# Optimization experiments

Measured on AMD Instinct MI355X. Metric: run time of the kernel, lower is better.

The kernel has to match this reference:

```python
import jax, jax.numpy as jnp
import numpy as np

B, S, HID, NH = 1, 2048, 2048, 16
HD = HID // NH
HALF = HD // 2
# quantization scales (registered buffers / pack() scales in the original module)
ATTN_IN_SCALE = 0.02   # attn_input_scale: dequant scale of int8 hidden_states
Q_OUT_SCALE = 0.05     # q_output_scale
K_OUT_SCALE = 0.05     # k_output_scale
V_OUT_SCALE = 0.04     # v_output_scale
Q_ROT_SCALE = 0.06     # q_rotary_output_scale
K_ROT_SCALE = 0.06     # k_rotary_output_scale
OUT_IN_SCALE = 0.03    # out_input_scale
W_ALPHA = 0.002        # folded int8 GEMM alpha for q/k/v W8A8B8O8Linear
BETA = 1.0             # bias scale of W8A8B8O8Linear
O_ALPHA = 0.001        # folded alpha for o_proj W8A8BFP32OFP32Linear
PROB_SCALE = 1.0 / 127.0  # attention-prob int8 quant scale
INV_SQRT_HD = float(1.0 / np.sqrt(HD))


def _q8(x):
    # saturating int8 quantization (values kept in float32)
    return jnp.clip(jnp.round(x), -127.0, 127.0)


def setup_inputs() -> dict:
    key = jax.random.key(0)
    ks = jax.random.split(key, 10)
    hidden_states = jax.random.normal(ks[0], (B, S, HID), jnp.float32)
    pos = jnp.arange(S, dtype=jnp.float32)
    inv_freq = 1.0 / (10000.0 ** (jnp.arange(0, HD, 2, dtype=jnp.float32) / HD))
    freqs = pos[:, None] * inv_freq[None, :]          # (S, HD//2)
    cos, sin = jnp.cos(freqs), jnp.sin(freqs)
    w8 = lambda k: jax.random.randint(k, (HID, HID), -127, 128).astype(jnp.float32)
    b8 = lambda k: jax.random.randint(k, (HID,), -127, 128).astype(jnp.float32)
    return dict(
        hidden_states=hidden_states, cos=cos, sin=sin,
        wq=w8(ks[1]), wk=w8(ks[2]), wv=w8(ks[3]), wo=w8(ks[4]),
        bq=b8(ks[5]), bk=b8(ks[6]), bv=b8(ks[7]),
        bo=jax.random.normal(ks[8], (HID,), jnp.float32) * 0.01,
    )


def reference(hidden_states, cos, sin, wq, wk, wv, wo, bq, bk, bv, bo):
    # quantize activations to int8 (done upstream of the module in smoothquant)
    x8 = _q8(hidden_states / ATTN_IN_SCALE)                       # (B,S,HID) int8 vals

    # W8A8B8O8Linear: int8 GEMM, alpha-scaled, int8 bias, saturate to int8
    def lin8(x, w, b):
        return _q8(jnp.einsum('bsi,oi->bso', x, w) * W_ALPHA + BETA * b)

    q8, k8, v8 = lin8(x8, wq, bq), lin8(x8, wk, bk), lin8(x8, wv, bv)

    # int8_rotary_embedding_fwd: dequant -> split-half rotary -> requant
    def rope(x8_flat, in_scale, out_scale):
        x = x8_flat.reshape(B, S, NH, HD) * in_scale
        x0, x1 = x[..., :HALF], x[..., HALF:]
        c, s_ = cos[None, :, None, :], sin[None, :, None, :]
        rot = jnp.concatenate([x0 * c - x1 * s_, x0 * s_ + x1 * c], axis=-1)
        return _q8(rot / out_scale)

    q = rope(q8, Q_OUT_SCALE, Q_ROT_SCALE)                        # (B,S,NH,HD)
    k = rope(k8, K_OUT_SCALE, K_ROT_SCALE)
    v = v8.reshape(B, S, NH, HD)

    # smooth_llama_context_attn_fwd: int8 QK^T -> fp32 scores -> causal softmax
    scores = jnp.einsum('bqhd,bkhd->bhqk', q, k) * (Q_ROT_SCALE * K_ROT_SCALE * INV_SQRT_HD)
    causal = jnp.tril(jnp.ones((S, S), bool))
    scores = jnp.where(causal[None, None], scores, -1e9)
    p = jax.nn.softmax(scores, axis=-1)
    p8 = _q8(p * 127.0)                                           # quantize probs to int8
    # int8 PV bmm, rescale and saturate to int8 for o_proj input
    o8 = _q8(jnp.einsum('bhqk,bkhd->bqhd', p8, v) * (PROB_SCALE * V_OUT_SCALE / OUT_IN_SCALE))
    o8 = o8.reshape(B, S, HID)

    # W8A8BFP32OFP32Linear: int8 GEMM, fp32 alpha + fp32 bias
    out = jnp.einsum('bso,po->bsp', o8, wo) * O_ALPHA + bo
    return out
```

## Files before the change

kernel.cpp:

```cpp
#include <hip/hip_runtime.h>
#include <math.h>

typedef __attribute__((ext_vector_type(4))) int i32x4;
typedef signed char s8;

constexpr int S   = 2048;
constexpr int HID = 2048;
constexpr int NH  = 16;
constexpr int HD  = 128;
constexpr int HALF = 64;

#define SCORE_SCALE ((float)(0.06 * 0.06 * 0.08838834764831845))
#define OSCALE      ((float)(((1.0 / 127.0) * 0.04) / 0.03))

__device__ __forceinline__ float clip127(float r){
  return fminf(fmaxf(r, -127.0f), 127.0f);
}
__device__ __forceinline__ i32x4 mfma_i8(i32x4 a, i32x4 b, i32x4 c){
  return __builtin_amdgcn_mfma_i32_16x16x64_i8(a, b, c, 0, 0, 0);
}
__device__ __forceinline__ void async16(const void* g, void* l){
  __builtin_amdgcn_global_load_lds(
      (const __attribute__((address_space(1))) unsigned*)g,
      (__attribute__((address_space(3))) unsigned*)l, 16, 0, 0);
}
template<int ROWS>
__device__ __forceinline__ void stage_async_swz(s8* dst, const s8* src, int stride){
  const int tid = threadIdx.x;
#pragma unroll
  for (int i = 0; i < ROWS/32; ++i){
    int o = i*256 + tid;
    int row = o >> 3, ch = o & 7;
    async16(src + (size_t)row*stride + ((ch ^ (row & 7))*16), dst + o*16);
  }
}
__device__ __forceinline__ i32x4 rd16(const s8* buf, int row, int ch){
  return *(const i32x4*)(buf + row*128 + ((ch ^ (row & 7))*16));
}
template<int ROWS>
__device__ __forceinline__ void stage64(s8* dst, const s8* src, int stride){
  const int tid = threadIdx.x;
#pragma unroll
  for (int i = 0; i < ROWS/64; ++i){
    int o = i*256 + tid;
    int row = o >> 2, slot = o & 3;
    int ch = slot ^ ((row >> 2) & 3);
    async16(src + (size_t)row*stride + ch*16, dst + o*16);
  }
}
__device__ __forceinline__ i32x4 rd64(const s8* buf, int row, int g){
  return *(const i32x4*)(buf + row*64 + ((g ^ ((row >> 2) & 3))*16));
}
__device__ __forceinline__ int tri_qt(int t){
  int qt = (int)((sqrtf(8.f*t + 1.f) - 1.f)*0.5f);
  while ((qt+1)*(qt+2)/2 <= t) ++qt;
  while (qt*(qt+1)/2 > t) --qt;
  return qt;
}

__global__ void cvt_all(const float* __restrict__ hid, const float* __restrict__ wq,
                        const float* __restrict__ wk, const float* __restrict__ wv,
                        const float* __restrict__ wo, s8* __restrict__ xd,
                        s8* __restrict__ qd, s8* __restrict__ kd,
                        s8* __restrict__ vd, s8* __restrict__ od, int n){
  const float* srcs[5] = {hid, wq, wk, wv, wo};
  s8* dsts[5] = {xd, qd, kd, vd, od};
  int which = blockIdx.y;
  const float* src = srcs[which];
  s8* dst = dsts[which];
  int i = (blockIdx.x * blockDim.x + threadIdx.x) * 4;
  if (i >= n) return;
  float4 v = *(const float4*)(src + i);
  float x[4] = {v.x, v.y, v.z, v.w};
  unsigned packed = 0;
#pragma unroll
  for (int j = 0; j < 4; ++j){
    int b;
    if (which == 0) b = (int)clip127(rintf(x[j] / 0.02f));
    else            b = (int)x[j];
    packed |= ((unsigned)(b & 255)) << (8*j);
  }
  *(unsigned*)(dst + i) = packed;
}

__global__ __launch_bounds__(256)
void gemm_qkv(const s8* __restrict__ A, const s8* __restrict__ W,
              const float* __restrict__ bq, const float* __restrict__ bk,
              const float* __restrict__ bv, s8* __restrict__ Out){
#pragma clang fp contract(off)
  constexpr int Kd = 2048, N = 2048, NT = 32;
  const int z = blockIdx.z;
  const s8* Bt = W + (size_t)z*(4u<<20);
  s8* Y = Out + (size_t)z*(4u<<20);
  const float* bss[3] = {bq, bk, bv};
  const float* bias = bss[z];
  __shared__ __attribute__((aligned(16))) s8 As[3][128*64];
  __shared__ __attribute__((aligned(16))) s8 Bs[3][128*64];
  const int lin = blockIdx.x + (blockIdx.y << 4);
  const int virt = (lin & 7)*32 + (lin >> 3);
  const int bm = virt & 15, bn = virt >> 4;
  const int tid = threadIdx.x;
  const int wid = tid >> 6, lane = tid & 63;
  const int wm = wid >> 1, wn = wid & 1;
  const int col16 = lane & 15, g = lane >> 4;
  i32x4 acc[4][4] = {};
  const s8* Ab = A + (size_t)(bm*128)*Kd;
  const s8* Bb = Bt + (size_t)(bn*128)*Kd;

  stage64<128>(As[0], Ab, Kd);       stage64<128>(Bs[0], Bb, Kd);
  stage64<128>(As[1], Ab + 64, Kd);  stage64<128>(Bs[1], Bb + 64, Kd);
  asm volatile("s_waitcnt vmcnt(4)" ::: "memory");
  __builtin_amdgcn_s_barrier();

  for (int T = 0; T < NT; ++T){
    const int nxt = T + 2;
    if (nxt < NT){
      stage64<128>(As[nxt%3], Ab + nxt*64, Kd);
      stage64<128>(Bs[nxt%3], Bb + nxt*64, Kd);
    }
    const s8* as = As[T%3];
    const s8* bs = Bs[T%3];
    i32x4 af[4], bf[4];
#pragma unroll
    for (int i = 0; i < 4; ++i) af[i] = rd64(as, wm*64 + i*16 + col16, g);
#pragma unroll
    for (int j = 0; j < 4; ++j) bf[j] = rd64(bs, wn*64 + j*16 + col16, g);
#pragma unroll
    for (int i = 0; i < 4; ++i)
#pragma unroll
      for (int j = 0; j < 4; ++j)
        acc[i][j] = mfma_i8(af[i], bf[j], acc[i][j]);
    if (nxt < NT) asm volatile("s_waitcnt vmcnt(4)" ::: "memory");
    else          asm volatile("s_waitcnt vmcnt(0)" ::: "memory");
    __builtin_amdgcn_s_barrier();
  }

#pragma unroll
  for (int i = 0; i < 4; ++i){
#pragma unroll
    for (int j = 0; j < 4; ++j){
      int row0 = bm*128 + wm*64 + i*16 + g*4;
      int col  = bn*128 + wn*64 + j*16 + col16;
#pragma unroll
      for (int r = 0; r < 4; ++r){
        float t = (float)acc[i][j][r] * 0.002f;
        t = t + bias[col];
        Y[(size_t)(row0 + r)*N + col] = (s8)(int)clip127(rintf(t));
      }
    }
  }
}

__global__ __launch_bounds__(256)
void gemm_o(const s8* __restrict__ A, const s8* __restrict__ Bt,
            const float* __restrict__ bias, float* __restrict__ Y){
#pragma clang fp contract(off)
  constexpr int Kd = 2048, N = 2048, NT = 32;
  __shared__ __attribute__((aligned(16))) s8 As[3][128*64];
  __shared__ __attribute__((aligned(16))) s8 Bs[3][64*64];
  const int lin = blockIdx.x + (blockIdx.y << 4);
  const int virt = (lin & 7)*64 + (lin >> 3);
  const int bm = virt & 15, bn = virt >> 4;
  const int tid = threadIdx.x;
  const int wid = tid >> 6, lane = tid & 63;
  const int wm = wid >> 1, wn = wid & 1;
  const int col16 = lane & 15, g = lane >> 4;
  i32x4 acc[4][2] = {};
  const s8* Ab = A + (size_t)(bm*128)*Kd;
  const s8* Bb = Bt + (size_t)(bn*64)*Kd;

  stage64<128>(As[0], Ab, Kd);       stage64<64>(Bs[0], Bb, Kd);
  stage64<128>(As[1], Ab + 64, Kd);  stage64<64>(Bs[1], Bb + 64, Kd);
  asm volatile("s_waitcnt vmcnt(3)" ::: "memory");
  __builtin_amdgcn_s_barrier();

  for (int T = 0; T < NT; ++T){
    const int nxt = T + 2;
    if (nxt < NT){
      stage64<128>(As[nxt%3], Ab + nxt*64, Kd);
      stage64<64>(Bs[nxt%3], Bb + nxt*64, Kd);
    }
    const s8* as = As[T%3];
    const s8* bs = Bs[T%3];
    i32x4 af[4], bf[2];
#pragma unroll
    for (int i = 0; i < 4; ++i) af[i] = rd64(as, wm*64 + i*16 + col16, g);
#pragma unroll
    for (int j = 0; j < 2; ++j) bf[j] = rd64(bs, wn*32 + j*16 + col16, g);
#pragma unroll
    for (int i = 0; i < 4; ++i)
#pragma unroll
      for (int j = 0; j < 2; ++j)
        acc[i][j] = mfma_i8(af[i], bf[j], acc[i][j]);
    if (nxt < NT) asm volatile("s_waitcnt vmcnt(3)" ::: "memory");
    else          asm volatile("s_waitcnt vmcnt(0)" ::: "memory");
    __builtin_amdgcn_s_barrier();
  }

#pragma unroll
  for (int i = 0; i < 4; ++i){
#pragma unroll
    for (int j = 0; j < 2; ++j){
      int row0 = bm*128 + wm*64 + i*16 + g*4;
      int col  = bn*64 + wn*32 + j*16 + col16;
#pragma unroll
      for (int r = 0; r < 4; ++r){
        float t = (float)acc[i][j][r] * 0.001f;
        t = t + bias[col];
        Y[(size_t)(row0 + r)*N + col] = t;
      }
    }
  }
}

__global__ void rope_qk(s8* __restrict__ q, s8* __restrict__ k,
                        const float* __restrict__ cosp, const float* __restrict__ sinp){
#pragma clang fp contract(off)
  int idx = blockIdx.x * blockDim.x + threadIdx.x;
  int t4 = (idx & 15) * 4;
  int h  = (idx >> 4) & (NH-1);
  int s  = idx >> 8;
  if (s >= S) return;
  float4 c4 = *(const float4*)(cosp + s*HALF + t4);
  float4 s4 = *(const float4*)(sinp + s*HALF + t4);
  float cc[4] = {c4.x, c4.y, c4.z, c4.w}, ss[4] = {s4.x, s4.y, s4.z, s4.w};
  int base = s*HID + h*HD + t4;
  {
    int a0 = *(const int*)(q + base), a1 = *(const int*)(q + base + HALF);
    unsigned o0 = 0, o1 = 0;
#pragma unroll
    for (int j = 0; j < 4; ++j){
      float x0 = (float)((s8)(a0 >> (8*j))) * 0.05f;
      float x1 = (float)((s8)(a1 >> (8*j))) * 0.05f;
      float r0 = x0*cc[j] - x1*ss[j];
      float r1 = x0*ss[j] + x1*cc[j];
      o0 |= ((unsigned)(((int)clip127(rintf(r0 / 0.06f))) & 255)) << (8*j);
      o1 |= ((unsigned)(((int)clip127(rintf(r1 / 0.06f))) & 255)) << (8*j);
    }
    *(unsigned*)(q + base) = o0; *(unsigned*)(q + base + HALF) = o1;
  }
  {
    int a0 = *(const int*)(k + base), a1 = *(const int*)(k + base + HALF);
    unsigned o0 = 0, o1 = 0;
#pragma unroll
    for (int j = 0; j < 4; ++j){
      float x0 = (float)((s8)(a0 >> (8*j))) * 0.05f;
      float x1 = (float)((s8)(a1 >> (8*j))) * 0.05f;
      float r0 = x0*cc[j] - x1*ss[j];
      float r1 = x0*ss[j] + x1*cc[j];
      o0 |= ((unsigned)(((int)clip127(rintf(r0 / 0.06f))) & 255)) << (8*j);
      o1 |= ((unsigned)(((int)clip127(rintf(r1 / 0.06f))) & 255)) << (8*j);
    }
    *(unsigned*)(k + base) = o0; *(unsigned*)(k + base + HALF) = o1;
  }
}

__global__ void vtrans(const s8* __restrict__ v, s8* __restrict__ vt){
  __shared__ __attribute__((aligned(16))) s8 t[128*144];
  int s0 = blockIdx.x * 128, h = blockIdx.y;
  int tid = threadIdx.x;
#pragma unroll
  for (int i = 0; i < 4; ++i){
    int vv = i*256 + tid, r = vv >> 3, ch = vv & 7;
    *(i32x4*)(t + r*144 + ch*16) = *(const i32x4*)(v + (size_t)(s0 + r)*HID + h*HD + ch*16);
  }
  __syncthreads();
#pragma unroll
  for (int i = 0; i < 4; ++i){
    int vv = i*256 + tid, d = vv >> 3, sc = (vv & 7)*16;
    s8 tmp[16];
#pragma unroll
    for (int j = 0; j < 16; ++j) tmp[j] = t[(sc + j)*144 + d];
    *(i32x4*)(vt + (size_t)(h*HD + d)*S + s0 + sc) = *(i32x4*)tmp;
  }
}

__global__ __launch_bounds__(256)
void attn_stats(const s8* __restrict__ qr, const s8* __restrict__ kr,
                float2* __restrict__ stats){
  const int x = blockIdx.x, h = blockIdx.y;
  const int tri = x >> 1, half = x & 1;
  const int qt = tri_qt(tri);
  const int kt = tri - qt*(qt+1)/2;
  const int q0 = qt*128 + half*64;
  const int tid = threadIdx.x, wid = tid >> 6, lane = tid & 63;
  const int col16 = lane & 15, g = lane >> 4;
  __shared__ __attribute__((aligned(16))) s8 Ks[128*128];

  stage_async_swz<128>(Ks, kr + (size_t)(kt*128)*HID + h*HD, HID);
  const s8* qb = qr + (size_t)(q0 + wid*16 + col16)*HID + h*HD + g*16;
  i32x4 aq[2];
  aq[0] = *(const i32x4*)(qb);
  aq[1] = *(const i32x4*)(qb + 64);
  __syncthreads();

  i32x4 sc[8] = {};
#pragma unroll
  for (int kk = 0; kk < 2; ++kk){
#pragma unroll
    for (int j = 0; j < 8; ++j){
      i32x4 bk = rd16(Ks, j*16 + col16, kk*4 + g);
      sc[j] = mfma_i8(aq[kk], bk, sc[j]);
    }
  }

  const bool diag = (kt == qt);
#pragma unroll
  for (int r = 0; r < 4; ++r){
    int rit = half*64 + wid*16 + g*4 + r;
    int qrow = qt*128 + rit;
    int mi = (int)0x80000000;
#pragma unroll
    for (int j = 0; j < 8; ++j){
      int v = sc[j][r];
      if (diag && (kt*128 + j*16 + col16 > qrow)) v = (int)0x80000000;
      mi = max(mi, v);
    }
    mi = max(mi, __shfl_xor(mi, 1));
    mi = max(mi, __shfl_xor(mi, 2));
    mi = max(mi, __shfl_xor(mi, 4));
    mi = max(mi, __shfl_xor(mi, 8));
    float mf = (float)mi * SCORE_SCALE;
    float st = 0.f;
#pragma unroll
    for (int j = 0; j < 8; ++j){
      float arg;
      if (diag && (kt*128 + j*16 + col16 > qrow)) arg = -1e30f;
      else arg = (float)sc[j][r] * SCORE_SCALE - mf;
      st += __expf(arg);
    }
    st += __shfl_xor(st, 1);
    st += __shfl_xor(st, 2);
    st += __shfl_xor(st, 4);
    st += __shfl_xor(st, 8);
    if (col16 == 0) stats[(size_t)(h*136 + tri)*128 + rit] = make_float2(mf, st);
  }
}

__global__ void attn_reduce(const float2* __restrict__ stats, float2* __restrict__ ml){
  const int row = threadIdx.x, qt = blockIdx.x, h = blockIdx.y;
  const int tri = qt*(qt+1)/2;
  float m = -3.0e38f;
  for (int kt = 0; kt <= qt; ++kt)
    m = fmaxf(m, stats[(size_t)(h*136 + tri + kt)*128 + row].x);
  float l = 0.f;
  for (int kt = 0; kt <= qt; ++kt){
    float2 s = stats[(size_t)(h*136 + tri + kt)*128 + row];
    l += s.y * __expf(s.x - m);
  }
  ml[(h*16 + qt)*128 + row] = make_float2(m, l);
}

__global__ __launch_bounds__(256)
void attn_score(const s8* __restrict__ qr, const s8* __restrict__ kr,
                const float2* __restrict__ ml, s8* __restrict__ P8){
  const int x = blockIdx.x, h = blockIdx.y;
  const int tri = x >> 1, half = x & 1;
  const int qt = tri_qt(tri);
  const int kt = tri - qt*(qt+1)/2;
  const int q0 = qt*128 + half*64;
  const int tid = threadIdx.x, wid = tid >> 6, lane = tid & 63;
  const int col16 = lane & 15, g = lane >> 4;
  __shared__ __attribute__((aligned(16))) s8 Ks[128*128];
  __shared__ __attribute__((aligned(16))) s8 Pl[64*128];

  stage_async_swz<128>(Ks, kr + (size_t)(kt*128)*HID + h*HD, HID);
  const s8* qb = qr + (size_t)(q0 + wid*16 + col16)*HID + h*HD + g*16;
  i32x4 aq[2];
  aq[0] = *(const i32x4*)(qb);
  aq[1] = *(const i32x4*)(qb + 64);
  float m[4], c[4];
#pragma unroll
  for (int r = 0; r < 4; ++r){
    float2 t = ml[(h*16 + qt)*128 + half*64 + wid*16 + g*4 + r];
    m[r] = t.x;
    c[r] = 127.0f / t.y;
  }
  __syncthreads();

  const bool diag = (kt == qt);
#pragma unroll
  for (int j = 0; j < 8; ++j){
    i32x4 s0 = {};
    s0 = mfma_i8(aq[0], rd16(Ks, j*16 + col16, g), s0);
    s0 = mfma_i8(aq[1], rd16(Ks, j*16 + col16, 4 + g), s0);
    int colk = j*16 + col16;
#pragma unroll
    for (int r = 0; r < 4; ++r){
      int row = wid*16 + g*4 + r;
      int qrow = q0 + row;
      float p8v = 0.0f;
      if (!diag || (kt*128 + colk) <= qrow){
        float sv = (float)s0[r] * SCORE_SCALE;
        p8v = clip127(rintf(__expf(sv - m[r]) * c[r]));
      }
      Pl[row*128 + colk] = (s8)(int)p8v;
    }
  }
  __syncthreads();
  s8* dst = P8 + (size_t)(h*136 + tri)*16384 + half*8192;
#pragma unroll
  for (int i = 0; i < 2; ++i){
    int o = i*256 + tid;
    *(i32x4*)(dst + o*16) = *(const i32x4*)(Pl + o*16);
  }
}

__global__ __launch_bounds__(256)
void attn_pv(const s8* __restrict__ P8, const s8* __restrict__ vt8,
             s8* __restrict__ o8){
  const int qt = 15 - blockIdx.x;
  const int h = blockIdx.y, dh = blockIdx.z;
  const int tri = qt*(qt+1)/2;
  const int nt = qt + 1;
  const int tid = threadIdx.x, wid = tid >> 6, lane = tid & 63;
  const int wm = wid >> 1, wn = wid & 1;
  const int col16 = lane & 15, g = lane >> 4;
  __shared__ __attribute__((aligned(16))) s8 Ps[3][128*128];
  __shared__ __attribute__((aligned(16))) s8 Vs[3][64*128];

#define PV_STAGE(t) do{ \
    stage_async_swz<128>(Ps[(t)%3], P8 + (size_t)(h*136 + tri + (t))*16384, 128); \
    stage_async_swz<64>(Vs[(t)%3], vt8 + (size_t)(h*HD + dh*64)*S + (t)*128, S); \
  }while(0)

  i32x4 acc[4][2] = {};
  PV_STAGE(0);
  if (nt > 1) PV_STAGE(1);
  if (nt > 1) asm volatile("s_waitcnt vmcnt(6)" ::: "memory");
  else        asm volatile("s_waitcnt vmcnt(0)" ::: "memory");
  __builtin_amdgcn_s_barrier();

  for (int T = 0; T < nt; ++T){
    const int nxt = T + 2;
    if (nxt < nt) PV_STAGE(nxt);
    const s8* ps = Ps[T%3];
    const s8* vs = Vs[T%3];
#pragma unroll
    for (int kk = 0; kk < 2; ++kk){
      i32x4 af[4], bf[2];
#pragma unroll
      for (int i = 0; i < 4; ++i) af[i] = rd16(ps, wm*64 + i*16 + col16, kk*4 + g);
#pragma unroll
      for (int j = 0; j < 2; ++j) bf[j] = rd16(vs, wn*32 + j*16 + col16, kk*4 + g);
#pragma unroll
      for (int i = 0; i < 4; ++i)
#pragma unroll
        for (int j = 0; j < 2; ++j)
          acc[i][j] = mfma_i8(af[i], bf[j], acc[i][j]);
    }
    if (nxt < nt) asm volatile("s_waitcnt vmcnt(6)" ::: "memory");
    else          asm volatile("s_waitcnt vmcnt(0)" ::: "memory");
    __builtin_amdgcn_s_barrier();
  }
#undef PV_STAGE

#pragma unroll
  for (int i = 0; i < 4; ++i)
#pragma unroll
    for (int j = 0; j < 2; ++j)
#pragma unroll
      for (int r = 0; r < 4; ++r){
        int row = qt*128 + wm*64 + i*16 + g*4 + r;
        int d = dh*64 + wn*32 + j*16 + col16;
        o8[(size_t)row*HID + h*HD + d] = (s8)(int)clip127(rintf((float)acc[i][j][r] * OSCALE));
      }
}

extern "C" void kernel_launch(void* const* d_in, const int* in_sizes, int n_in,
                              void* d_out, int out_size, void* d_ws, size_t ws_size,
                              hipStream_t stream) {
  const float* hidden = (const float*)d_in[0];
  const float* cosp   = (const float*)d_in[1];
  const float* sinp   = (const float*)d_in[2];
  const float* wq     = (const float*)d_in[3];
  const float* wk     = (const float*)d_in[4];
  const float* wv     = (const float*)d_in[5];
  const float* wo     = (const float*)d_in[6];
  const float* bq     = (const float*)d_in[7];
  const float* bk     = (const float*)d_in[8];
  const float* bv     = (const float*)d_in[9];
  const float* bo     = (const float*)d_in[10];
  float* out = (float*)d_out;

  const size_t MB = 1024*1024;
  s8* ws8 = (s8*)d_ws;
  s8* x8  = ws8 + 0*MB;
  s8* wq8 = ws8 + 4*MB;
  s8* wk8 = ws8 + 8*MB;
  s8* wv8 = ws8 + 12*MB;
  s8* wo8 = ws8 + 16*MB;
  s8* q8  = ws8 + 20*MB;
  s8* k8  = ws8 + 24*MB;
  s8* v8  = ws8 + 28*MB;
  s8* vt8 = ws8 + 32*MB;
  s8* P8  = ws8 + 36*MB;
  s8* o8  = x8;
  float2* stats = (float2*)(ws8 + 4*MB);
  float2* mlb   = (float2*)(ws8 + 4*MB + 2400*1024);

  const int n = HID*HID;
  dim3 b256(256);

  cvt_all<<<dim3(n/1024, 5), b256, 0, stream>>>(hidden, wq, wk, wv, wo,
                                                x8, wq8, wk8, wv8, wo8, n);

  gemm_qkv<<<dim3(16, 16, 3), b256, 0, stream>>>(x8, wq8, bq, bk, bv, q8);

  rope_qk<<<(S*NH*16)/256, b256, 0, stream>>>(q8, k8, cosp, sinp);
  vtrans<<<dim3(S/128, NH), b256, 0, stream>>>(v8, vt8);

  attn_stats<<<dim3(272, 16), b256, 0, stream>>>(q8, k8, stats);
  attn_reduce<<<dim3(16, 16), dim3(128), 0, stream>>>(stats, mlb);
  attn_score<<<dim3(272, 16), b256, 0, stream>>>(q8, k8, mlb, P8);
  attn_pv<<<dim3(16, 16, 2), b256, 0, stream>>>(P8, vt8, o8);

  gemm_o<<<dim3(16, 32), b256, 0, stream>>>(o8, wo8, bo, out);
}
```

Baseline: 147.2 us.

## Fuse rope with V transpose, fold softmax reduce into score, simplify PV loop

Merges the rope and V-transpose kernels into a single launch that dispatches on block index, and removes the attn_reduce kernel by having each attn_score block recompute the row max and sum from the per-tile stats. The PV kernel drops its triple-buffered async prefetch pipeline in favour of a single-buffer load, sync, compute loop. Fewer launches cut launch and inter-kernel gaps, but every score block now redundantly re-reads up to 16 stats per row. The PV kernel also loses load/compute overlap, though its smaller LDS footprint may raise occupancy.

```diff
diff --git a/kernel.cpp b/kernel.cpp
--- a/kernel.cpp
+++ b/kernel.cpp
@@ -213,65 +213,67 @@
   }
 }
 
-__global__ void rope_qk(s8* __restrict__ q, s8* __restrict__ k,
-                        const float* __restrict__ cosp, const float* __restrict__ sinp){
+__global__ void rope_vtrans(s8* __restrict__ q, s8* __restrict__ k,
+                            const float* __restrict__ cosp, const float* __restrict__ sinp,
+                            const s8* __restrict__ v, s8* __restrict__ vt){
 #pragma clang fp contract(off)
-  int idx = blockIdx.x * blockDim.x + threadIdx.x;
-  int t4 = (idx & 15) * 4;
-  int h  = (idx >> 4) & (NH-1);
-  int s  = idx >> 8;
-  if (s >= S) return;
-  float4 c4 = *(const float4*)(cosp + s*HALF + t4);
-  float4 s4 = *(const float4*)(sinp + s*HALF + t4);
-  float cc[4] = {c4.x, c4.y, c4.z, c4.w}, ss[4] = {s4.x, s4.y, s4.z, s4.w};
-  int base = s*HID + h*HD + t4;
-  {
-    int a0 = *(const int*)(q + base), a1 = *(const int*)(q + base + HALF);
-    unsigned o0 = 0, o1 = 0;
-#pragma unroll
-    for (int j = 0; j < 4; ++j){
-      float x0 = (float)((s8)(a0 >> (8*j))) * 0.05f;
-      float x1 = (float)((s8)(a1 >> (8*j))) * 0.05f;
-      float r0 = x0*cc[j] - x1*ss[j];
-      float r1 = x0*ss[j] + x1*cc[j];
-      o0 |= ((unsigned)(((int)clip127(rintf(r0 / 0.06f))) & 255)) << (8*j);
-      o1 |= ((unsigned)(((int)clip127(rintf(r1 / 0.06f))) & 255)) << (8*j);
-    }
-    *(unsigned*)(q + base) = o0; *(unsigned*)(q + base + HALF) = o1;
-  }
-  {
-    int a0 = *(const int*)(k + base), a1 = *(const int*)(k + base + HALF);
-    unsigned o0 = 0, o1 = 0;
-#pragma unroll
-    for (int j = 0; j < 4; ++j){
-      float x0 = (float)((s8)(a0 >> (8*j))) * 0.05f;
-      float x1 = (float)((s8)(a1 >> (8*j))) * 0.05f;
-      float r0 = x0*cc[j] - x1*ss[j];
-      float r1 = x0*ss[j] + x1*cc[j];
-      o0 |= ((unsigned)(((int)clip127(rintf(r0 / 0.06f))) & 255)) << (8*j);
-      o1 |= ((unsigned)(((int)clip127(rintf(r1 / 0.06f))) & 255)) << (8*j);
-    }
-    *(unsigned*)(k + base) = o0; *(unsigned*)(k + base + HALF) = o1;
-  }
-}
-
-__global__ void vtrans(const s8* __restrict__ v, s8* __restrict__ vt){
   __shared__ __attribute__((aligned(16))) s8 t[128*144];
-  int s0 = blockIdx.x * 128, h = blockIdx.y;
-  int tid = threadIdx.x;
-#pragma unroll
-  for (int i = 0; i < 4; ++i){
-    int vv = i*256 + tid, r = vv >> 3, ch = vv & 7;
-    *(i32x4*)(t + r*144 + ch*16) = *(const i32x4*)(v + (size_t)(s0 + r)*HID + h*HD + ch*16);
-  }
-  __syncthreads();
-#pragma unroll
-  for (int i = 0; i < 4; ++i){
-    int vv = i*256 + tid, d = vv >> 3, sc = (vv & 7)*16;
-    s8 tmp[16];
-#pragma unroll
-    for (int j = 0; j < 16; ++j) tmp[j] = t[(sc + j)*144 + d];
-    *(i32x4*)(vt + (size_t)(h*HD + d)*S + s0 + sc) = *(i32x4*)tmp;
+  const int bx = blockIdx.x, tid = threadIdx.x;
+  if (bx < 2048){
+    int idx = bx * 256 + tid;
+    int t4 = (idx & 15) * 4;
+    int h  = (idx >> 4) & (NH-1);
+    int s  = idx >> 8;
+    if (s >= S) return;
+    float4 c4 = *(const float4*)(cosp + s*HALF + t4);
+    float4 s4 = *(const float4*)(sinp + s*HALF + t4);
+    float cc[4] = {c4.x, c4.y, c4.z, c4.w}, ss[4] = {s4.x, s4.y, s4.z, s4.w};
+    int base = s*HID + h*HD + t4;
+    {
+      int a0 = *(const int*)(q + base), a1 = *(const int*)(q + base + HALF);
+      unsigned o0 = 0, o1 = 0;
+#pragma unroll
+      for (int j = 0; j < 4; ++j){
+        float x0 = (float)((s8)(a0 >> (8*j))) * 0.05f;
+        float x1 = (float)((s8)(a1 >> (8*j))) * 0.05f;
+        float r0 = x0*cc[j] - x1*ss[j];
+        float r1 = x0*ss[j] + x1*cc[j];
+        o0 |= ((unsigned)(((int)clip127(rintf(r0 / 0.06f))) & 255)) << (8*j);
+        o1 |= ((unsigned)(((int)clip127(rintf(r1 / 0.06f))) & 255)) << (8*j);
+      }
+      *(unsigned*)(q + base) = o0; *(unsigned*)(q + base + HALF) = o1;
+    }
+    {
+      int a0 = *(const int*)(k + base), a1 = *(const int*)(k + base + HALF);
+      unsigned o0 = 0, o1 = 0;
+#pragma unroll
+      for (int j = 0; j < 4; ++j){
+        float x0 = (float)((s8)(a0 >> (8*j))) * 0.05f;
+        float x1 = (float)((s8)(a1 >> (8*j))) * 0.05f;
+        float r0 = x0*cc[j] - x1*ss[j];
+        float r1 = x0*ss[j] + x1*cc[j];
+        o0 |= ((unsigned)(((int)clip127(rintf(r0 / 0.06f))) & 255)) << (8*j);
+        o1 |= ((unsigned)(((int)clip127(rintf(r1 / 0.06f))) & 255)) << (8*j);
+      }
+      *(unsigned*)(k + base) = o0; *(unsigned*)(k + base + HALF) = o1;
+    }
+  } else {
+    const int rem = bx - 2048;
+    const int s0 = (rem & 15) * 128, h = rem >> 4;
+#pragma unroll
+    for (int i = 0; i < 4; ++i){
+      int vv = i*256 + tid, r = vv >> 3, ch = vv & 7;
+      *(i32x4*)(t + r*144 + ch*16) = *(const i32x4*)(v + (size_t)(s0 + r)*HID + h*HD + ch*16);
+    }
+    __syncthreads();
+#pragma unroll
+    for (int i = 0; i < 4; ++i){
+      int vv = i*256 + tid, d = vv >> 3, sc = (vv & 7)*16;
+      s8 tmp[16];
+#pragma unroll
+      for (int j = 0; j < 16; ++j) tmp[j] = t[(sc + j)*144 + d];
+      *(i32x4*)(vt + (size_t)(h*HD + d)*S + s0 + sc) = *(i32x4*)tmp;
+    }
   }
 }
 
@@ -337,27 +339,14 @@
   }
 }
 
-__global__ void attn_reduce(const float2* __restrict__ stats, float2* __restrict__ ml){
-  const int row = threadIdx.x, qt = blockIdx.x, h = blockIdx.y;
-  const int tri = qt*(qt+1)/2;
-  float m = -3.0e38f;
-  for (int kt = 0; kt <= qt; ++kt)
-    m = fmaxf(m, stats[(size_t)(h*136 + tri + kt)*128 + row].x);
-  float l = 0.f;
-  for (int kt = 0; kt <= qt; ++kt){
-    float2 s = stats[(size_t)(h*136 + tri + kt)*128 + row];
-    l += s.y * __expf(s.x - m);
-  }
-  ml[(h*16 + qt)*128 + row] = make_float2(m, l);
-}
-
 __global__ __launch_bounds__(256)
 void attn_score(const s8* __restrict__ qr, const s8* __restrict__ kr,
-                const float2* __restrict__ ml, s8* __restrict__ P8){
+                const float2* __restrict__ stats, s8* __restrict__ P8){
   const int x = blockIdx.x, h = blockIdx.y;
   const int tri = x >> 1, half = x & 1;
   const int qt = tri_qt(tri);
   const int kt = tri - qt*(qt+1)/2;
+  const int tri0 = qt*(qt+1)/2;
   const int q0 = qt*128 + half*64;
   const int tid = threadIdx.x, wid = tid >> 6, lane = tid & 63;
   const int col16 = lane & 15, g = lane >> 4;
@@ -369,12 +358,21 @@
   i32x4 aq[2];
   aq[0] = *(const i32x4*)(qb);
   aq[1] = *(const i32x4*)(qb + 64);
+  const float2* st = stats + (size_t)(h*136)*128;
   float m[4], c[4];
 #pragma unroll
   for (int r = 0; r < 4; ++r){
-    float2 t = ml[(h*16 + qt)*128 + half*64 + wid*16 + g*4 + r];
-    m[r] = t.x;
-    c[r] = 127.0f / t.y;
+    int row = half*64 + wid*16 + g*4 + r;
+    float mm = -3.0e38f;
+    for (int k2 = 0; k2 <= qt; ++k2)
+      mm = fmaxf(mm, st[(size_t)(tri0 + k2)*128 + row].x);
+    float ll = 0.f;
+    for (int k2 = 0; k2 <= qt; ++k2){
+      float2 s2 = st[(size_t)(tri0 + k2)*128 + row];
+      ll += s2.y * __expf(s2.x - mm);
+    }
+    m[r] = mm;
+    c[r] = 127.0f / ll;
   }
   __syncthreads();
 
@@ -412,49 +410,32 @@
   const int qt = 15 - blockIdx.x;
   const int h = blockIdx.y, dh = blockIdx.z;
   const int tri = qt*(qt+1)/2;
-  const int nt = qt + 1;
   const int tid = threadIdx.x, wid = tid >> 6, lane = tid & 63;
   const int wm = wid >> 1, wn = wid & 1;
   const int col16 = lane & 15, g = lane >> 4;
-  __shared__ __attribute__((aligned(16))) s8 Ps[3][128*128];
-  __shared__ __attribute__((aligned(16))) s8 Vs[3][64*128];
-
-#define PV_STAGE(t) do{ \
-    stage_async_swz<128>(Ps[(t)%3], P8 + (size_t)(h*136 + tri + (t))*16384, 128); \
-    stage_async_swz<64>(Vs[(t)%3], vt8 + (size_t)(h*HD + dh*64)*S + (t)*128, S); \
-  }while(0)
+  __shared__ __attribute__((aligned(16))) s8 Ps[128*128];
+  __shared__ __attribute__((aligned(16))) s8 Vs[64*128];
 
   i32x4 acc[4][2] = {};
-  PV_STAGE(0);
-  if (nt > 1) PV_STAGE(1);
-  if (nt > 1) asm volatile("s_waitcnt vmcnt(6)" ::: "memory");
-  else        asm volatile("s_waitcnt vmcnt(0)" ::: "memory");
-  __builtin_amdgcn_s_barrier();
-
-  for (int T = 0; T < nt; ++T){
-    const int nxt = T + 2;
-    if (nxt < nt) PV_STAGE(nxt);
-    const s8* ps = Ps[T%3];
-    const s8* vs = Vs[T%3];
+  for (int kt = 0; kt <= qt; ++kt){
+    stage_async_swz<128>(Ps, P8 + (size_t)(h*136 + tri + kt)*16384, 128);
+    stage_async_swz<64>(Vs, vt8 + (size_t)(h*HD + dh*64)*S + kt*128, S);
+    __syncthreads();
 #pragma unroll
     for (int kk = 0; kk < 2; ++kk){
       i32x4 af[4], bf[2];
 #pragma unroll
-      for (int i = 0; i < 4; ++i) af[i] = rd16(ps, wm*64 + i*16 + col16, kk*4 + g);
-#pragma unroll
-      for (int j = 0; j < 2; ++j) bf[j] = rd16(vs, wn*32 + j*16 + col16, kk*4 + g);
+      for (int i = 0; i < 4; ++i) af[i] = rd16(Ps, wm*64 + i*16 + col16, kk*4 + g);
+#pragma unroll
+      for (int j = 0; j < 2; ++j) bf[j] = rd16(Vs, wn*32 + j*16 + col16, kk*4 + g);
 #pragma unroll
       for (int i = 0; i < 4; ++i)
 #pragma unroll
         for (int j = 0; j < 2; ++j)
           acc[i][j] = mfma_i8(af[i], bf[j], acc[i][j]);
     }
-    if (nxt < nt) asm volatile("s_waitcnt vmcnt(6)" ::: "memory");
-    else          asm volatile("s_waitcnt vmcnt(0)" ::: "memory");
-    __builtin_amdgcn_s_barrier();
-  }
-#undef PV_STAGE
-
+    __syncthreads();
+  }
 #pragma unroll
   for (int i = 0; i < 4; ++i)
 #pragma unroll
@@ -497,7 +478,6 @@
   s8* P8  = ws8 + 36*MB;
   s8* o8  = x8;
   float2* stats = (float2*)(ws8 + 4*MB);
-  float2* mlb   = (float2*)(ws8 + 4*MB + 2400*1024);
 
   const int n = HID*HID;
   dim3 b256(256);
@@ -507,12 +487,10 @@
 
   gemm_qkv<<<dim3(16, 16, 3), b256, 0, stream>>>(x8, wq8, bq, bk, bv, q8);
 
-  rope_qk<<<(S*NH*16)/256, b256, 0, stream>>>(q8, k8, cosp, sinp);
-  vtrans<<<dim3(S/128, NH), b256, 0, stream>>>(v8, vt8);
+  rope_vtrans<<<2304, b256, 0, stream>>>(q8, k8, cosp, sinp, v8, vt8);
 
   attn_stats<<<dim3(272, 16), b256, 0, stream>>>(q8, k8, stats);
-  attn_reduce<<<dim3(16, 16), dim3(128), 0, stream>>>(stats, mlb);
-  attn_score<<<dim3(272, 16), b256, 0, stream>>>(q8, k8, mlb, P8);
+  attn_score<<<dim3(272, 16), b256, 0, stream>>>(q8, k8, stats, P8);
   attn_pv<<<dim3(16, 16, 2), b256, 0, stream>>>(P8, vt8, o8);
 
   gemm_o<<<dim3(16, 32), b256, 0, stream>>>(o8, wo8, bo, out);
```

New measurement: 181.6 us. 1.23x slower.
